# Kernel optimization log

Hardware: AMD Instinct MI355X
Metric: run time of the kernel (lower is better)

Reference implementation:

```python
import jax, jax.numpy as jnp
import numpy as np

TOP_K = 2

def setup_inputs() -> dict:
    key = jax.random.key(0)
    k0, k1, k2, k3, k4 = jax.random.split(key, 5)
    B, S, D, H, E = 2, 2048, 1024, 2048, 8
    x = jax.random.normal(k0, (B, S, D), dtype=jnp.float32)
    router_w = jax.random.normal(k1, (D, E), dtype=jnp.float32) * (1.0 / np.sqrt(D))
    wg = jax.random.normal(k2, (E, D, H), dtype=jnp.float32) * (1.0 / np.sqrt(D))
    wu = jax.random.normal(k3, (E, D, H), dtype=jnp.float32) * (1.0 / np.sqrt(D))
    wd = jax.random.normal(k4, (E, H, D), dtype=jnp.float32) * (1.0 / np.sqrt(H))
    return {"x": x, "router_w": router_w, "wg": wg, "wu": wu, "wd": wd}

def reference(x, router_w, wg, wu, wd):
    B, S, D = x.shape
    E = router_w.shape[1]
    xf = x.reshape(-1, D)                                   # [T, D]
    router_logits = xf @ router_w                           # [T, E]
    top_logits, top_idx = jax.lax.top_k(router_logits, TOP_K)
    top_w = jax.nn.softmax(top_logits, axis=-1)             # [T, k]
    # Dense combine weights: W[t, e] = routing weight if e in top-k of t, else 0.
    combine = jnp.sum(jax.nn.one_hot(top_idx, E, dtype=x.dtype) * top_w[..., None], axis=1)  # [T, E]
    # SwiGLU experts, computed for all tokens and masked by the combine weights
    # (mathematically identical to the gather/scatter form in the original).
    gate = jnp.einsum('td,edh->eth', xf, wg)                # [E, T, H]
    up = jnp.einsum('td,edh->eth', xf, wu)                  # [E, T, H]
    fused = jax.nn.silu(gate) * up                          # [E, T, H]
    expert_out = jnp.einsum('eth,ehd->etd', fused, wd)      # [E, T, D]
    y = jnp.einsum('etd,te->td', expert_out, combine)       # [T, D]
    return y.reshape(B, S, D)
```

## Files before the change

kernel.cpp:

```cpp
#include <hip/hip_runtime.h>
#include <hip/hip_bf16.h>

#define T_TOK 4096
#define DDIM  1024
#define HDIM  2048
#define NEXP  8
#define MAXSLOT 9216

typedef __attribute__((ext_vector_type(4))) float f32x4;
typedef __attribute__((ext_vector_type(8))) short s16x8;
typedef __hip_bfloat16 bf16;

typedef const void __attribute__((address_space(1))) gvoid;
typedef void __attribute__((address_space(3))) svoid;

__device__ __forceinline__ void gload16(const void* g, void* l) {
    __builtin_amdgcn_global_load_lds((gvoid*)g, (svoid*)l, 16, 0, 0);
}

__global__ void router_cast_kernel(const float* __restrict__ x, const float* __restrict__ rw,
                                   int* __restrict__ r_e, float* __restrict__ r_w,
                                   bf16* __restrict__ xb) {
    int wave = threadIdx.x >> 6, lane = threadIdx.x & 63;
    int t = blockIdx.x * 4 + wave;
    const float* xr = x + (size_t)t * DDIM;
    bf16* xbr = xb + (size_t)t * DDIM;
    double acc[NEXP];
#pragma unroll
    for (int e = 0; e < NEXP; ++e) acc[e] = 0.0;
#pragma unroll
    for (int c = 0; c < 4; ++c) {
        int d = c * 256 + lane * 4;
        float4 v = *reinterpret_cast<const float4*>(xr + d);
        union { ushort4 u; bf16 h[4]; } o;
        o.h[0] = __float2bfloat16(v.x);
        o.h[1] = __float2bfloat16(v.y);
        o.h[2] = __float2bfloat16(v.z);
        o.h[3] = __float2bfloat16(v.w);
        *reinterpret_cast<ushort4*>(xbr + d) = o.u;
        const float* rw0 = rw + (size_t)d * NEXP;
#pragma unroll
        for (int j = 0; j < 4; ++j) {
            float xv = (&v.x)[j];
            const float* rwr = rw0 + j * NEXP;
#pragma unroll
            for (int e = 0; e < NEXP; ++e) acc[e] += (double)xv * (double)rwr[e];
        }
    }
#pragma unroll
    for (int e = 0; e < NEXP; ++e) {
#pragma unroll
        for (int off = 32; off > 0; off >>= 1) acc[e] += __shfl_down(acc[e], off);
    }
    if (lane == 0) {
        int i0 = 0; double v0 = acc[0];
#pragma unroll
        for (int e = 1; e < NEXP; ++e) if (acc[e] > v0) { v0 = acc[e]; i0 = e; }
        int i1 = -1; double v1 = -1e300;
#pragma unroll
        for (int e = 0; e < NEXP; ++e) { if (e == i0) continue; if (acc[e] > v1) { v1 = acc[e]; i1 = e; } }
        float w0 = 1.0f / (1.0f + expf((float)(v1 - v0)));
        float w1 = 1.0f - w0;
        r_e[2*t]   = i0; r_e[2*t+1] = i1;
        r_w[2*t]   = w0; r_w[2*t+1] = w1;
    }
}

__global__ void binning_kernel(const int* __restrict__ r_e, const float* __restrict__ r_w,
                               int* __restrict__ offs, int* __restrict__ cnt,
                               int* __restrict__ list, float* __restrict__ slot_w) {
    __shared__ int scnt[NEXP], scur[NEXP], soff[NEXP + 1];
    int tid = threadIdx.x;
    if (tid < NEXP) { scnt[tid] = 0; scur[tid] = 0; }
    __syncthreads();
    for (int i = tid; i < 2 * T_TOK; i += 512) atomicAdd(&scnt[r_e[i]], 1);
    __syncthreads();
    if (tid == 0) {
        int s = 0;
        for (int e = 0; e < NEXP; ++e) { soff[e] = s; s += (scnt[e] + 127) & ~127; }
        soff[NEXP] = s;
    }
    __syncthreads();
    if (tid < NEXP + 1) offs[tid] = soff[tid];
    if (tid < NEXP) cnt[tid] = scnt[tid];
    for (int i = tid; i < 2 * T_TOK; i += 512) {
        int e = r_e[i];
        int pos = atomicAdd(&scur[e], 1);
        int slot = soff[e] + pos;
        list[slot] = i >> 1;
        slot_w[slot] = r_w[i];
    }
}

__global__ void transpose_gu_kernel(const float* __restrict__ wg, const float* __restrict__ wu,
                                    bf16* __restrict__ wguT) {
    __shared__ bf16 tile[64][68];
    int which = blockIdx.z >> 3;
    int e = blockIdx.z & 7;
    const float* inp = (which ? wu : wg) + (size_t)e * DDIM * HDIM;
    bf16* outp = wguT + (size_t)e * 2 * HDIM * DDIM;
    int r0 = blockIdx.x * 64, c0 = blockIdx.y * 64;
    int tid = threadIdx.x;
#pragma unroll
    for (int i = 0; i < 4; ++i) {
        int idx = i * 256 + tid;
        int r = idx >> 4, c4 = (idx & 15) * 4;
        float4 v = *reinterpret_cast<const float4*>(inp + (size_t)(r0 + r) * HDIM + c0 + c4);
        union { ushort4 u; bf16 h[4]; } o;
        o.h[0] = __float2bfloat16(v.x);
        o.h[1] = __float2bfloat16(v.y);
        o.h[2] = __float2bfloat16(v.z);
        o.h[3] = __float2bfloat16(v.w);
        *reinterpret_cast<ushort4*>(&tile[r][c4]) = o.u;
    }
    __syncthreads();
#pragma unroll
    for (int i = 0; i < 4; ++i) {
        int idx = i * 256 + tid;
        int c = idx >> 4, r4 = (idx & 15) * 4;
        union { ushort4 u; bf16 h[4]; } w;
        w.h[0] = tile[r4 + 0][c];
        w.h[1] = tile[r4 + 1][c];
        w.h[2] = tile[r4 + 2][c];
        w.h[3] = tile[r4 + 3][c];
        *reinterpret_cast<ushort4*>(outp + ((size_t)(c0 + c) * 2 + which) * DDIM + r0 + r4) = w.u;
    }
}

__global__ void transpose_wd_kernel(const float* __restrict__ wd, bf16* __restrict__ wdT) {
    __shared__ bf16 tile[64][68];
    const float* inp = wd + (size_t)blockIdx.z * HDIM * DDIM;
    bf16* outp = wdT + (size_t)blockIdx.z * DDIM * HDIM;
    int r0 = blockIdx.x * 64, c0 = blockIdx.y * 64;
    int tid = threadIdx.x;
#pragma unroll
    for (int i = 0; i < 4; ++i) {
        int idx = i * 256 + tid;
        int r = idx >> 4, c4 = (idx & 15) * 4;
        float4 v = *reinterpret_cast<const float4*>(inp + (size_t)(r0 + r) * DDIM + c0 + c4);
        union { ushort4 u; bf16 h[4]; } o;
        o.h[0] = __float2bfloat16(v.x);
        o.h[1] = __float2bfloat16(v.y);
        o.h[2] = __float2bfloat16(v.z);
        o.h[3] = __float2bfloat16(v.w);
        *reinterpret_cast<ushort4*>(&tile[r][c4]) = o.u;
    }
    __syncthreads();
#pragma unroll
    for (int i = 0; i < 4; ++i) {
        int idx = i * 256 + tid;
        int c = idx >> 4, r4 = (idx & 15) * 4;
        union { ushort4 u; bf16 h[4]; } w;
        w.h[0] = tile[r4 + 0][c];
        w.h[1] = tile[r4 + 1][c];
        w.h[2] = tile[r4 + 2][c];
        w.h[3] = tile[r4 + 3][c];
        *reinterpret_cast<ushort4*>(outp + (size_t)(c0 + c) * HDIM + r0 + r4) = w.u;
    }
}

__device__ __forceinline__ int find_expert(const int* offs, int slot0) {
    int e = 0;
#pragma unroll
    for (int i = 0; i < NEXP - 1; ++i) e += (offs[e + 1] <= slot0) ? 1 : 0;
    return e;
}

__global__ __launch_bounds__(512, 2)
void gateup_kernel(const bf16* __restrict__ xb, const bf16* __restrict__ wguT,
                   const int* __restrict__ offs, const int* __restrict__ cnt,
                   const int* __restrict__ list, bf16* __restrict__ hbuf) {
    int slot0 = blockIdx.y * 128;
    if (slot0 >= offs[NEXP]) return;
    int e = find_expert(offs, slot0);
    int base = offs[e];
    int ne = cnt[e];
    int m0 = slot0 - base;
    int n0 = blockIdx.x * 128;

    __shared__ bf16 As[2][8192];
    __shared__ bf16 Bs[2][8192];

    int tid = threadIdx.x, lane = tid & 63, wid = tid >> 6;
    int sub = lane >> 3;
    int koff = 8 * ((lane & 7) ^ sub);

    const bf16* bbase = wguT + (size_t)e * (2 * HDIM) * DDIM + (size_t)n0 * DDIM;

    const bf16* aS[2]; const bf16* bS[2];
    int sdst[2];
#pragma unroll
    for (int j = 0; j < 2; ++j) {
        int q = wid + j * 8;
        int row = q * 8 + sub;
        int r = m0 + row; if (r > ne - 1) r = ne - 1;
        aS[j] = xb + (size_t)list[base + r] * DDIM + koff;
        bS[j] = bbase + (size_t)row * DDIM + koff;
        sdst[j] = q * 512;
    }

    int rl = lane & 15, kq = 8 * (lane >> 4);
    int wrow = (wid >> 2) * 64;
    int wcol = (wid & 3) * 32;
    int xorv = (rl & 7) * 8;

    f32x4 zero4 = {0.f, 0.f, 0.f, 0.f};
    f32x4 acc[4][2];
#pragma unroll
    for (int mi = 0; mi < 4; ++mi) { acc[mi][0] = zero4; acc[mi][1] = zero4; }

    const int nk = DDIM / 64;

#define GU_STAGE(tt, buf)                                     \
    {                                                         \
        int k0 = (tt) * 64;                                   \
        gload16(aS[0] + k0, &As[buf][sdst[0]]);               \
        gload16(aS[1] + k0, &As[buf][sdst[1]]);               \
        gload16(bS[0] + k0, &Bs[buf][sdst[0]]);               \
        gload16(bS[1] + k0, &Bs[buf][sdst[1]]);               \
    }

#define GU_COMPUTE(Ab, Bb)                                                        \
    _Pragma("unroll")                                                             \
    for (int kk = 0; kk < 2; ++kk) {                                              \
        int kos = (kk * 32 + kq) ^ xorv;                                          \
        s16x8 a[4], b[2];                                                         \
        _Pragma("unroll")                                                         \
        for (int mi = 0; mi < 4; ++mi)                                            \
            a[mi] = *reinterpret_cast<const s16x8*>(&(Ab)[(wrow + mi * 16 + rl) * 64 + kos]); \
        _Pragma("unroll")                                                         \
        for (int ni = 0; ni < 2; ++ni)                                            \
            b[ni] = *reinterpret_cast<const s16x8*>(&(Bb)[(wcol + ni * 16 + rl) * 64 + kos]); \
        __builtin_amdgcn_s_setprio(1);                                            \
        _Pragma("unroll")                                                         \
        for (int mi = 0; mi < 4; ++mi)                                            \
            _Pragma("unroll")                                                     \
            for (int ni = 0; ni < 2; ++ni)                                        \
                acc[mi][ni] = __builtin_amdgcn_mfma_f32_16x16x32_bf16(a[mi], b[ni], acc[mi][ni], 0, 0, 0); \
        __builtin_amdgcn_s_setprio(0);                                            \
    }

    GU_STAGE(0, 0);
    GU_STAGE(1, 1);

    for (int t = 0; t < nk; ++t) {
        if (t + 1 < nk) asm volatile("s_waitcnt vmcnt(4)" ::: "memory");
        else            asm volatile("s_waitcnt vmcnt(0)" ::: "memory");
        __builtin_amdgcn_s_barrier();
        GU_COMPUTE(As[t & 1], Bs[t & 1]);
        __builtin_amdgcn_sched_barrier(0);
        __builtin_amdgcn_s_barrier();
        if (t + 2 < nk) GU_STAGE(t + 2, t & 1);
    }
#undef GU_COMPUTE
#undef GU_STAGE

    int rbase = (lane >> 4) * 4, cbase = lane & 15;
    bool evenlane = (lane & 1) == 0;
#pragma unroll
    for (int mi = 0; mi < 4; ++mi) {
#pragma unroll
        for (int ni = 0; ni < 2; ++ni) {
#pragma unroll
            for (int r = 0; r < 4; ++r) {
                float own = acc[mi][ni][r];
                float oth = __shfl_xor(own, 1);
                int row = m0 + wrow + mi * 16 + rbase + r;
                if (evenlane && row < ne) {
                    float g = own, u = oth;
                    float h = (g / (1.0f + expf(-g))) * u;
                    int hcol = (n0 + wcol + ni * 16 + cbase) >> 1;
                    hbuf[(size_t)(base + row) * HDIM + hcol] = __float2bfloat16(h);
                }
            }
        }
    }
}

__global__ __launch_bounds__(512, 2)
void down_kernel(const bf16* __restrict__ hbuf, const bf16* __restrict__ wdT,
                 const int* __restrict__ offs, const int* __restrict__ cnt,
                 const int* __restrict__ list, const float* __restrict__ slot_w,
                 float* __restrict__ y) {
    int slot0 = blockIdx.y * 128;
    if (slot0 >= offs[NEXP]) return;
    int e = find_expert(offs, slot0);
    int base = offs[e];
    int ne = cnt[e];
    int m0 = slot0 - base;
    int n0 = blockIdx.x * 128;

    __shared__ bf16 As[2][8192];
    __shared__ bf16 Bs[2][8192];

    int tid = threadIdx.x, lane = tid & 63, wid = tid >> 6;
    int sub = lane >> 3;
    int koff = 8 * ((lane & 7) ^ sub);

    const bf16* bbase = wdT + (size_t)e * DDIM * HDIM + (size_t)n0 * HDIM;

    const bf16* aS[2]; const bf16* bS[2];
    int sdst[2];
#pragma unroll
    for (int j = 0; j < 2; ++j) {
        int q = wid + j * 8;
        int row = q * 8 + sub;
        int r = m0 + row; if (r > ne - 1) r = ne - 1;
        aS[j] = hbuf + (size_t)(base + r) * HDIM + koff;
        bS[j] = bbase + (size_t)row * HDIM + koff;
        sdst[j] = q * 512;
    }

    int rl = lane & 15, kq = 8 * (lane >> 4);
    int wrow = (wid >> 2) * 64;
    int wcol = (wid & 3) * 32;
    int xorv = (rl & 7) * 8;

    f32x4 zero4 = {0.f, 0.f, 0.f, 0.f};
    f32x4 acc[4][2];
#pragma unroll
    for (int mi = 0; mi < 4; ++mi) { acc[mi][0] = zero4; acc[mi][1] = zero4; }

    const int nk = HDIM / 64;

#define DN_STAGE(tt, buf)                                     \
    {                                                         \
        int k0 = (tt) * 64;                                   \
        gload16(aS[0] + k0, &As[buf][sdst[0]]);               \
        gload16(aS[1] + k0, &As[buf][sdst[1]]);               \
        gload16(bS[0] + k0, &Bs[buf][sdst[0]]);               \
        gload16(bS[1] + k0, &Bs[buf][sdst[1]]);               \
    }

#define DN_COMPUTE(Ab, Bb)                                                        \
    _Pragma("unroll")                                                             \
    for (int kk = 0; kk < 2; ++kk) {                                              \
        int kos = (kk * 32 + kq) ^ xorv;                                          \
        s16x8 a[4], b[2];                                                         \
        _Pragma("unroll")                                                         \
        for (int mi = 0; mi < 4; ++mi)                                            \
            a[mi] = *reinterpret_cast<const s16x8*>(&(Ab)[(wrow + mi * 16 + rl) * 64 + kos]); \
        _Pragma("unroll")                                                         \
        for (int ni = 0; ni < 2; ++ni)                                            \
            b[ni] = *reinterpret_cast<const s16x8*>(&(Bb)[(wcol + ni * 16 + rl) * 64 + kos]); \
        __builtin_amdgcn_s_setprio(1);                                            \
        _Pragma("unroll")                                                         \
        for (int mi = 0; mi < 4; ++mi)                                            \
            _Pragma("unroll")                                                     \
            for (int ni = 0; ni < 2; ++ni)                                        \
                acc[mi][ni] = __builtin_amdgcn_mfma_f32_16x16x32_bf16(a[mi], b[ni], acc[mi][ni], 0, 0, 0); \
        __builtin_amdgcn_s_setprio(0);                                            \
    }

    DN_STAGE(0, 0);
    DN_STAGE(1, 1);

    for (int t = 0; t < nk; ++t) {
        if (t + 1 < nk) asm volatile("s_waitcnt vmcnt(4)" ::: "memory");
        else            asm volatile("s_waitcnt vmcnt(0)" ::: "memory");
        __builtin_amdgcn_s_barrier();
        DN_COMPUTE(As[t & 1], Bs[t & 1]);
        __builtin_amdgcn_sched_barrier(0);
        __builtin_amdgcn_s_barrier();
        if (t + 2 < nk) DN_STAGE(t + 2, t & 1);
    }
#undef DN_COMPUTE
#undef DN_STAGE

    int rbase = (lane >> 4) * 4, cbase = lane & 15;
#pragma unroll
    for (int mi = 0; mi < 4; ++mi) {
#pragma unroll
        for (int r = 0; r < 4; ++r) {
            int row = m0 + wrow + mi * 16 + rbase + r;
            if (row < ne) {
                int slot = base + row;
                int tok = list[slot];
                float w = slot_w[slot];
                float* yrow = y + (size_t)tok * DDIM + n0 + wcol + cbase;
#pragma unroll
                for (int ni = 0; ni < 2; ++ni)
                    atomicAdd(yrow + ni * 16, w * acc[mi][ni][r]);
            }
        }
    }
}

extern "C" void kernel_launch(void* const* d_in, const int* in_sizes, int n_in,
                              void* d_out, int out_size, void* d_ws, size_t ws_size,
                              hipStream_t stream) {
    const float* x  = (const float*)d_in[0];
    const float* rw = (const float*)d_in[1];
    const float* wg = (const float*)d_in[2];
    const float* wu = (const float*)d_in[3];
    const float* wd = (const float*)d_in[4];
    float* y = (float*)d_out;

    char* ws = (char*)d_ws;
    int*   r_e    = (int*)  (ws + 0);
    float* r_w    = (float*)(ws + 32768);
    int*   offs   = (int*)  (ws + 65600);
    int*   cnt    = (int*)  (ws + 65640);
    int*   list   = (int*)  (ws + 65792);
    float* slot_w = (float*)(ws + 65792 + 4 * MAXSLOT);
    bf16*  xb     = (bf16*) (ws + 1048576ull);
    bf16*  wguT   = (bf16*) (ws + 16777216ull);
    bf16*  wdT    = (bf16*) (ws + 83886080ull);
    bf16*  hbuf   = (bf16*) (ws + 117440512ull);

    transpose_gu_kernel<<<dim3(DDIM / 64, HDIM / 64, 2 * NEXP), 256, 0, stream>>>(wg, wu, wguT);
    transpose_wd_kernel<<<dim3(HDIM / 64, DDIM / 64, NEXP), 256, 0, stream>>>(wd, wdT);

    router_cast_kernel<<<dim3(T_TOK / 4), 256, 0, stream>>>(x, rw, r_e, r_w, xb);
    binning_kernel<<<dim3(1), 512, 0, stream>>>(r_e, r_w, offs, cnt, list, slot_w);

    hipMemsetAsync(d_out, 0, (size_t)out_size * sizeof(float), stream);

    gateup_kernel<<<dim3(2 * HDIM / 128, MAXSLOT / 128, 1), 512, 0, stream>>>(
        xb, wguT, offs, cnt, list, hbuf);
    down_kernel<<<dim3(DDIM / 128, MAXSLOT / 128, 1), 512, 0, stream>>>(
        hbuf, wdT, offs, cnt, list, slot_w, y);
}
```

Before: 284.1 us.

## Merge weight transposes into one launch, swizzle LDS tile, fold output zeroing

```diff
diff --git a/kernel.cpp b/kernel.cpp
--- a/kernel.cpp
+++ b/kernel.cpp
@@ -20,7 +20,14 @@
 
 __global__ void router_cast_kernel(const float* __restrict__ x, const float* __restrict__ rw,
                                    int* __restrict__ r_e, float* __restrict__ r_w,
-                                   bf16* __restrict__ xb) {
+                                   bf16* __restrict__ xb, float* __restrict__ y) {
+    {
+        float4 z4 = {0.f, 0.f, 0.f, 0.f};
+        size_t ybase = (size_t)blockIdx.x * 4096 + threadIdx.x * 4;
+#pragma unroll
+        for (int i = 0; i < 4; ++i)
+            *reinterpret_cast<float4*>(y + ybase + (size_t)i * 1024) = z4;
+    }
     int wave = threadIdx.x >> 6, lane = threadIdx.x & 63;
     int t = blockIdx.x * 4 + wave;
     const float* xr = x + (size_t)t * DDIM;
@@ -92,70 +99,59 @@
     }
 }
 
-__global__ void transpose_gu_kernel(const float* __restrict__ wg, const float* __restrict__ wu,
-                                    bf16* __restrict__ wguT) {
-    __shared__ bf16 tile[64][68];
-    int which = blockIdx.z >> 3;
-    int e = blockIdx.z & 7;
-    const float* inp = (which ? wu : wg) + (size_t)e * DDIM * HDIM;
-    bf16* outp = wguT + (size_t)e * 2 * HDIM * DDIM;
-    int r0 = blockIdx.x * 64, c0 = blockIdx.y * 64;
+__device__ __forceinline__ int sw_r(int r) { return ((r >> 2) ^ ((r & 3) << 2)) & 15; }
+
+__global__ void transpose_all_kernel(const float* __restrict__ wg, const float* __restrict__ wu,
+                                     const float* __restrict__ wd,
+                                     bf16* __restrict__ wguT, bf16* __restrict__ wdT) {
+    __shared__ __align__(16) bf16 tile[64 * 64];
+    int bid = blockIdx.x;
+    const float* inp; bf16* outp; int C, OS, r0, c0;
+    if (bid < 8192) {
+        int z = bid >> 9;
+        int t = bid & 511;
+        int which = z >> 3, e = z & 7;
+        inp = (which ? wu : wg) + (size_t)e * DDIM * HDIM;
+        outp = wguT + (size_t)e * 2 * HDIM * DDIM + (size_t)which * DDIM;
+        C = HDIM; OS = 2 * DDIM;
+        r0 = (t >> 5) * 64;
+        c0 = (t & 31) * 64;
+    } else {
+        int b2 = bid - 8192;
+        int e = b2 >> 9;
+        int t = b2 & 511;
+        inp = wd + (size_t)e * HDIM * DDIM;
+        outp = wdT + (size_t)e * DDIM * HDIM;
+        C = DDIM; OS = HDIM;
+        r0 = (t >> 4) * 64;
+        c0 = (t & 15) * 64;
+    }
     int tid = threadIdx.x;
 #pragma unroll
     for (int i = 0; i < 4; ++i) {
         int idx = i * 256 + tid;
         int r = idx >> 4, c4 = (idx & 15) * 4;
-        float4 v = *reinterpret_cast<const float4*>(inp + (size_t)(r0 + r) * HDIM + c0 + c4);
+        float4 v = *reinterpret_cast<const float4*>(inp + (size_t)(r0 + r) * C + c0 + c4);
         union { ushort4 u; bf16 h[4]; } o;
         o.h[0] = __float2bfloat16(v.x);
         o.h[1] = __float2bfloat16(v.y);
         o.h[2] = __float2bfloat16(v.z);
         o.h[3] = __float2bfloat16(v.w);
-        *reinterpret_cast<ushort4*>(&tile[r][c4]) = o.u;
+        *reinterpret_cast<ushort4*>(&tile[r * 64 + 4 * ((c4 >> 2) ^ sw_r(r))]) = o.u;
     }
     __syncthreads();
 #pragma unroll
     for (int i = 0; i < 4; ++i) {
         int idx = i * 256 + tid;
         int c = idx >> 4, r4 = (idx & 15) * 4;
+        int g = c >> 2, ce = c & 3;
         union { ushort4 u; bf16 h[4]; } w;
-        w.h[0] = tile[r4 + 0][c];
-        w.h[1] = tile[r4 + 1][c];
-        w.h[2] = tile[r4 + 2][c];
-        w.h[3] = tile[r4 + 3][c];
-        *reinterpret_cast<ushort4*>(outp + ((size_t)(c0 + c) * 2 + which) * DDIM + r0 + r4) = w.u;
-    }
-}
-
-__global__ void transpose_wd_kernel(const float* __restrict__ wd, bf16* __restrict__ wdT) {
-    __shared__ bf16 tile[64][68];
-    const float* inp = wd + (size_t)blockIdx.z * HDIM * DDIM;
-    bf16* outp = wdT + (size_t)blockIdx.z * DDIM * HDIM;
-    int r0 = blockIdx.x * 64, c0 = blockIdx.y * 64;
-    int tid = threadIdx.x;
-#pragma unroll
-    for (int i = 0; i < 4; ++i) {
-        int idx = i * 256 + tid;
-        int r = idx >> 4, c4 = (idx & 15) * 4;
-        float4 v = *reinterpret_cast<const float4*>(inp + (size_t)(r0 + r) * DDIM + c0 + c4);
-        union { ushort4 u; bf16 h[4]; } o;
-        o.h[0] = __float2bfloat16(v.x);
-        o.h[1] = __float2bfloat16(v.y);
-        o.h[2] = __float2bfloat16(v.z);
-        o.h[3] = __float2bfloat16(v.w);
-        *reinterpret_cast<ushort4*>(&tile[r][c4]) = o.u;
-    }
-    __syncthreads();
-#pragma unroll
-    for (int i = 0; i < 4; ++i) {
-        int idx = i * 256 + tid;
-        int c = idx >> 4, r4 = (idx & 15) * 4;
-        union { ushort4 u; bf16 h[4]; } w;
-        w.h[0] = tile[r4 + 0][c];
-        w.h[1] = tile[r4 + 1][c];
-        w.h[2] = tile[r4 + 2][c];
-        w.h[3] = tile[r4 + 3][c];
-        *reinterpret_cast<ushort4*>(outp + (size_t)(c0 + c) * HDIM + r0 + r4) = w.u;
+#pragma unroll
+        for (int j = 0; j < 4; ++j) {
+            int r = r4 + j;
+            w.h[j] = tile[r * 64 + 4 * (g ^ sw_r(r)) + ce];
+        }
+        *reinterpret_cast<ushort4*>(outp + (size_t)(c0 + c) * OS + r0 + r4) = w.u;
     }
 }
 
@@ -408,13 +404,10 @@
     bf16*  wdT    = (bf16*) (ws + 83886080ull);
     bf16*  hbuf   = (bf16*) (ws + 117440512ull);
 
-    transpose_gu_kernel<<<dim3(DDIM / 64, HDIM / 64, 2 * NEXP), 256, 0, stream>>>(wg, wu, wguT);
-    transpose_wd_kernel<<<dim3(HDIM / 64, DDIM / 64, NEXP), 256, 0, stream>>>(wd, wdT);
-
-    router_cast_kernel<<<dim3(T_TOK / 4), 256, 0, stream>>>(x, rw, r_e, r_w, xb);
+    transpose_all_kernel<<<dim3(12288), 256, 0, stream>>>(wg, wu, wd, wguT, wdT);
+
+    router_cast_kernel<<<dim3(T_TOK / 4), 256, 0, stream>>>(x, rw, r_e, r_w, xb, y);
     binning_kernel<<<dim3(1), 512, 0, stream>>>(r_e, r_w, offs, cnt, list, slot_w);
-
-    hipMemsetAsync(d_out, 0, (size_t)out_size * sizeof(float), stream);
 
     gateup_kernel<<<dim3(2 * HDIM / 128, MAXSLOT / 128, 1), 512, 0, stream>>>(
         xb, wguT, offs, cnt, list, hbuf);
```

New measurement: 278.0 us. 1.02x faster.
